# Performance work log

Hardware: AMD Instinct MI355X
Metric: run time of the kernel (lower is better)

The kernel has to match this reference:

```python
import jax, jax.numpy as jnp
from jax import lax
import numpy as np


def _dilate3x3(img):
    # Faithful to torch: zero-pad by 1 (f.pad default), then 3x3 max over the
    # padded window (strel of ones => plain max, zeros from padding included).
    imgp = jnp.pad(img, ((0, 0), (0, 0), (1, 1), (1, 1)))
    return lax.reduce_window(imgp, -jnp.inf, lax.max,
                             (1, 1, 3, 3), (1, 1, 1, 1), 'VALID')


def setup_inputs() -> dict:
    key = jax.random.key(0)
    x = jax.random.normal(key, (32, 3, 512, 512), dtype=jnp.float32)
    return {"in_tensor": x, "n_pixels": 20}


def reference(in_tensor, n_pixels):
    # smoother = linspace(1, 0, n+1); smoother_diff = -diff => 1/n per step (linear)
    smoother = jnp.linspace(1.0, 0.0, n_pixels + 1)
    sdiff = (-jnp.diff(smoother)).astype(in_tensor.dtype)  # [n_pixels]

    def step(carry, w):
        out, img = carry
        out = out + w * img
        img = _dilate3x3(img)
        return (out, img), None

    init = (jnp.zeros_like(in_tensor), in_tensor)
    (out, _), _ = lax.scan(step, init, sdiff)
    return out
```

## Files before the change

### kernel.cpp

```cpp
#include <hip/hip_runtime.h>

#define IMG_W 512
#define IMG_H 512
#define TILE 88
#define HALO 20
#define NSTEP 19
#define RH 8
#define RW 8
#define REG 128

__device__ __forceinline__ float max3f(float a, float b, float c) {
    return fmaxf(fmaxf(a, b), c);
}

__device__ __forceinline__ float dpp_shr1(float v) {
    int i = __builtin_bit_cast(int, v);
    i = __builtin_amdgcn_update_dpp(0, i, 0x111, 0xf, 0xf, true);
    return __builtin_bit_cast(float, i);
}
__device__ __forceinline__ float dpp_shl1(float v) {
    int i = __builtin_bit_cast(int, v);
    i = __builtin_amdgcn_update_dpp(0, i, 0x101, 0xf, 0xf, true);
    return __builtin_bit_cast(float, i);
}
__device__ __forceinline__ float bperm(int byteAddr, float v) {
    int i = __builtin_amdgcn_ds_bpermute(byteAddr, __builtin_bit_cast(int, v));
    return __builtin_bit_cast(float, i);
}

__device__ __forceinline__ void hrow(const float (&Ar)[RW], float (&h)[RW]) {
    float hl = dpp_shr1(Ar[RW - 1]);
    float hr = dpp_shl1(Ar[0]);
    h[0] = max3f(hl, Ar[0], Ar[1]);
    #pragma unroll
    for (int c = 1; c < RW - 1; ++c) h[c] = max3f(Ar[c - 1], Ar[c], Ar[c + 1]);
    h[RW - 1] = max3f(Ar[RW - 2], Ar[RW - 1], hr);
}

template<bool XM, bool YM>
__device__ __forceinline__ void rowop(const float (&hm1)[RW], const float (&hc)[RW],
                                      const float (&hn)[RW], float (&Ar)[RW],
                                      float (&accr)[RW], const float (&colm)[RW],
                                      float rm, bool needR) {
    float v[RW];
    #pragma unroll
    for (int c = 0; c < RW; ++c) v[c] = max3f(hm1[c], hc[c], hn[c]);
    if (XM) {
        #pragma unroll
        for (int c = 0; c < RW; ++c) v[c] *= colm[c];
    }
    if (YM) {
        if (needR) {
            #pragma unroll
            for (int c = 0; c < RW; ++c) v[c] *= rm;
        }
    }
    #pragma unroll
    for (int c = 0; c < RW; ++c) { Ar[c] = v[c]; accr[c] += v[c]; }
}

template<bool XM, bool YM>
__device__ __forceinline__ void body(const float* __restrict__ xc, float* __restrict__ oc,
                                     int gx0, int gy0, int tx, int ty, int lane,
                                     float4 (*botR)[4][16][2], float4 (*topR)[4][16][2]) {
    const int rx = tx * RW;
    const int ry = ty * RH;
    const int gx = gx0 + rx;
    const int gy = gy0 + ry;

    float A[RH][RW];
    float acc[RH][RW];
    float colm[RW], rowm[RH];
    bool needR = false;

    if (XM) {
        #pragma unroll
        for (int c = 0; c < RW; ++c) {
            int xx = gx + c;
            colm[c] = (xx >= 0 && xx < IMG_W) ? 1.f : 0.f;
        }
    }
    if (YM) {
        #pragma unroll
        for (int r = 0; r < RH; ++r) {
            int yy = gy + r;
            rowm[r] = (yy >= 0 && yy < IMG_H) ? 1.f : 0.f;
        }
        needR = (gy < 0) || (gy + RH > IMG_H);
    }

    if (XM || YM) {
        const bool fullin = (gx >= 0) && (gx + RW <= IMG_W) && (gy >= 0) && (gy + RH <= IMG_H);
        if (fullin) {
            #pragma unroll
            for (int r = 0; r < RH; ++r) {
                const float4* rp = (const float4*)(xc + (size_t)(gy + r) * IMG_W + gx);
                float4 v0 = rp[0], v1 = rp[1];
                A[r][0] = v0.x; A[r][1] = v0.y; A[r][2] = v0.z; A[r][3] = v0.w;
                A[r][4] = v1.x; A[r][5] = v1.y; A[r][6] = v1.z; A[r][7] = v1.w;
            }
        } else {
            #pragma unroll
            for (int r = 0; r < RH; ++r) {
                const int yr = gy + r;
                const int yy = min(max(yr, 0), IMG_H - 1);
                float rmv = (yr >= 0 && yr < IMG_H) ? 1.f : 0.f;
                const float* rp = xc + (size_t)yy * IMG_W;
                #pragma unroll
                for (int c = 0; c < RW; ++c) {
                    const int xr = gx + c;
                    const int xx = min(max(xr, 0), IMG_W - 1);
                    float m = rmv;
                    if (XM) m *= colm[c];
                    A[r][c] = rp[xx] * m;
                }
            }
        }
    } else {
        #pragma unroll
        for (int r = 0; r < RH; ++r) {
            const float4* rp = (const float4*)(xc + (size_t)(gy + r) * IMG_W + gx);
            float4 v0 = rp[0], v1 = rp[1];
            A[r][0] = v0.x; A[r][1] = v0.y; A[r][2] = v0.z; A[r][3] = v0.w;
            A[r][4] = v1.x; A[r][5] = v1.y; A[r][6] = v1.z; A[r][7] = v1.w;
        }
    }
    #pragma unroll
    for (int r = 0; r < RH; ++r) {
        #pragma unroll
        for (int c = 0; c < RW; ++c) acc[r][c] = A[r][c];
    }

    const int upA = ((lane - 16) & 63) << 2;
    const int dnA = ((lane + 16) & 63) << 2;
    const int gq = ty >> 2;
    const int tw = ty & 3;

    #pragma unroll 1
    for (int s = 0; s < NSTEP; ++s) {
        float hc[RW], h7[RW];
        hrow(A[0], hc);
        hrow(A[RH - 1], h7);
        float hm1[RW], hbot[RW];
        #pragma unroll
        for (int c = 0; c < RW; ++c) hm1[c] = bperm(upA, h7[c]);
        #pragma unroll
        for (int c = 0; c < RW; ++c) hbot[c] = bperm(dnA, hc[c]);

        const int buf = s & 1;
        if (tw == 3) {
            botR[buf][gq][tx][0] = make_float4(h7[0], h7[1], h7[2], h7[3]);
            botR[buf][gq][tx][1] = make_float4(h7[4], h7[5], h7[6], h7[7]);
        } else if (tw == 0) {
            topR[buf][gq][tx][0] = make_float4(hc[0], hc[1], hc[2], hc[3]);
            topR[buf][gq][tx][1] = make_float4(hc[4], hc[5], hc[6], hc[7]);
        }
        __syncthreads();
        if (tw == 0) {
            if (gq > 0) {
                float4 u0 = botR[buf][gq - 1][tx][0], u1 = botR[buf][gq - 1][tx][1];
                hm1[0] = u0.x; hm1[1] = u0.y; hm1[2] = u0.z; hm1[3] = u0.w;
                hm1[4] = u1.x; hm1[5] = u1.y; hm1[6] = u1.z; hm1[7] = u1.w;
            }
        } else if (tw == 3) {
            if (gq < 3) {
                float4 d0 = topR[buf][gq + 1][tx][0], d1 = topR[buf][gq + 1][tx][1];
                hbot[0] = d0.x; hbot[1] = d0.y; hbot[2] = d0.z; hbot[3] = d0.w;
                hbot[4] = d1.x; hbot[5] = d1.y; hbot[6] = d1.z; hbot[7] = d1.w;
            }
        }

        float h1[RW]; hrow(A[1], h1);
        float h2[RW]; hrow(A[2], h2);
        rowop<XM, YM>(hc, h1, h2, A[1], acc[1], colm, YM ? rowm[1] : 1.f, needR);
        rowop<XM, YM>(hm1, hc, h1, A[0], acc[0], colm, YM ? rowm[0] : 1.f, needR);
        float h3[RW]; hrow(A[3], h3);
        rowop<XM, YM>(h1, h2, h3, A[2], acc[2], colm, YM ? rowm[2] : 1.f, needR);
        float h4[RW]; hrow(A[4], h4);
        rowop<XM, YM>(h2, h3, h4, A[3], acc[3], colm, YM ? rowm[3] : 1.f, needR);
        float h5[RW]; hrow(A[5], h5);
        rowop<XM, YM>(h3, h4, h5, A[4], acc[4], colm, YM ? rowm[4] : 1.f, needR);
        float h6[RW]; hrow(A[6], h6);
        rowop<XM, YM>(h4, h5, h6, A[5], acc[5], colm, YM ? rowm[5] : 1.f, needR);
        rowop<XM, YM>(h5, h6, h7, A[6], acc[6], colm, YM ? rowm[6] : 1.f, needR);
        rowop<XM, YM>(h6, h7, hbot, A[7], acc[7], colm, YM ? rowm[7] : 1.f, needR);
    }

    if (XM || YM) {
        #pragma unroll
        for (int r = 0; r < RH; ++r) {
            const int rr = ry + r;
            const int yy = gy0 + rr;
            if (rr >= HALO && rr < HALO + TILE && yy < IMG_H) {
                #pragma unroll
                for (int c = 0; c < RW; ++c) {
                    const int cc = rx + c;
                    const int xx = gx0 + cc;
                    if (cc >= HALO && cc < HALO + TILE && xx < IMG_W)
                        oc[(size_t)yy * IMG_W + xx] = 0.05f * acc[r][c];
                }
            }
        }
    } else {
        #pragma unroll
        for (int r = 0; r < RH; ++r) {
            const int rr = ry + r;
            if (rr < HALO || rr >= HALO + TILE) continue;
            const int yy = gy0 + rr;
            float* rowp = oc + (size_t)yy * IMG_W + gx;
            if (tx >= 3 && tx <= 12) {
                ((float4*)rowp)[0] = make_float4(0.05f * acc[r][0], 0.05f * acc[r][1],
                                                 0.05f * acc[r][2], 0.05f * acc[r][3]);
                ((float4*)rowp)[1] = make_float4(0.05f * acc[r][4], 0.05f * acc[r][5],
                                                 0.05f * acc[r][6], 0.05f * acc[r][7]);
            } else if (tx == 2) {
                ((float4*)rowp)[1] = make_float4(0.05f * acc[r][4], 0.05f * acc[r][5],
                                                 0.05f * acc[r][6], 0.05f * acc[r][7]);
            } else if (tx == 13) {
                ((float4*)rowp)[0] = make_float4(0.05f * acc[r][0], 0.05f * acc[r][1],
                                                 0.05f * acc[r][2], 0.05f * acc[r][3]);
            }
        }
    }
}

__global__ __launch_bounds__(256, 2)
void blur_outwards_kernel(const float* __restrict__ x, float* __restrict__ out) {
    __shared__ float4 botR[2][4][16][2];
    __shared__ float4 topR[2][4][16][2];

    const int tid = threadIdx.x;
    const int tx = tid & 15;
    const int ty = tid >> 4;
    const int lane = tid & 63;

    const int ch  = blockIdx.z;
    const int gx0 = (int)blockIdx.x * TILE - HALO;
    const int gy0 = (int)blockIdx.y * TILE - HALO;

    const float* __restrict__ xc = x + (size_t)ch * (IMG_W * IMG_H);
    float* __restrict__ oc = out + (size_t)ch * (IMG_W * IMG_H);

    const bool xe = (gx0 < 0) || (gx0 + REG > IMG_W);
    const bool ye = (gy0 < 0) || (gy0 + REG > IMG_H);
    if (!xe && !ye)      body<false, false>(xc, oc, gx0, gy0, tx, ty, lane, botR, topR);
    else if (xe && !ye)  body<true,  false>(xc, oc, gx0, gy0, tx, ty, lane, botR, topR);
    else if (!xe && ye)  body<false, true >(xc, oc, gx0, gy0, tx, ty, lane, botR, topR);
    else                 body<true,  true >(xc, oc, gx0, gy0, tx, ty, lane, botR, topR);
}

extern "C" void kernel_launch(void* const* d_in, const int* in_sizes, int n_in,
                              void* d_out, int out_size, void* d_ws, size_t ws_size,
                              hipStream_t stream) {
    const float* x = (const float*)d_in[0];
    float* out = (float*)d_out;
    dim3 grid((IMG_W + TILE - 1) / TILE,
              (IMG_H + TILE - 1) / TILE,
              96);
    blur_outwards_kernel<<<grid, 256, 0, stream>>>(x, out);
}
```

Measured before the change: 313.9 us.

## Fuse two dilation steps per halo exchange to halve barriers and shuffles

Each loop iteration now exchanges a two-row halo (raw rows instead of horizontal maxima) and applies two 3x3 dilations back to back in registers, followed by one final single-step dilation, so 19 steps become 9 double steps plus 1. This halves the number of __syncthreads and halo exchange rounds. In exchange it does extra bpermutes and LDS traffic per round, recomputes the horizontal max for the halo rows, and adds register pressure from the larger halo buffers, which could reduce occupancy under the 2-blocks bound.

New measurement: 406.1 us. 29.4% more time.

```diff
diff --git a/kernel.cpp b/kernel.cpp
--- a/kernel.cpp
+++ b/kernel.cpp
@@ -4,7 +4,7 @@
 #define IMG_H 512
 #define TILE 88
 #define HALO 20
-#define NSTEP 19
+#define NSUP 9
 #define RH 8
 #define RW 8
 #define REG 128
@@ -38,31 +38,93 @@
 }
 
 template<bool XM, bool YM>
-__device__ __forceinline__ void rowop(const float (&hm1)[RW], const float (&hc)[RW],
-                                      const float (&hn)[RW], float (&Ar)[RW],
-                                      float (&accr)[RW], const float (&colm)[RW],
-                                      float rm, bool needR) {
-    float v[RW];
-    #pragma unroll
-    for (int c = 0; c < RW; ++c) v[c] = max3f(hm1[c], hc[c], hn[c]);
+__device__ __forceinline__ void drow(const float (&ha)[RW], const float (&hb)[RW],
+                                     const float (&hc)[RW], float (&d)[RW],
+                                     const float (&colm)[RW], float rm, bool needR) {
+    #pragma unroll
+    for (int c = 0; c < RW; ++c) d[c] = max3f(ha[c], hb[c], hc[c]);
     if (XM) {
         #pragma unroll
-        for (int c = 0; c < RW; ++c) v[c] *= colm[c];
+        for (int c = 0; c < RW; ++c) d[c] *= colm[c];
     }
     if (YM) {
         if (needR) {
             #pragma unroll
-            for (int c = 0; c < RW; ++c) v[c] *= rm;
-        }
-    }
-    #pragma unroll
-    for (int c = 0; c < RW; ++c) { Ar[c] = v[c]; accr[c] += v[c]; }
+            for (int c = 0; c < RW; ++c) d[c] *= rm;
+        }
+    }
+}
+
+template<bool XM, bool YM>
+__device__ __forceinline__ void dil2(float (&A)[RH][RW], float (&acc)[RH][RW],
+        const float (&Am2)[RW], const float (&Am1)[RW],
+        const float (&Ap8)[RW], const float (&Ap9)[RW],
+        const float (&colm)[RW], const float (&rowm)[RH],
+        float rmm1, float rm8, bool needR)
+{
+    float h1[3][RW], h2[3][RW];
+    hrow(A[0], h1[0]);
+    hrow(Am2, h1[1]);
+    hrow(Am1, h1[2]);
+    #pragma unroll
+    for (int i = 0; i <= 9; ++i) {
+        if (i >= 1) {
+            if (i <= 7)      hrow(A[i], h1[i % 3]);
+            else if (i == 8) hrow(Ap8, h1[2]);
+            else             hrow(Ap9, h1[0]);
+        }
+        {
+            const int rr = i - 1;
+            const int sa = (rr + 2) % 3;
+            const int sb = (rr + 3) % 3;
+            const int sc = i % 3;
+            float D1[RW];
+            const float rmv = YM ? ((rr == -1) ? rmm1
+                                  : ((rr == 8) ? rm8
+                                  : rowm[(rr >= 0 && rr <= 7) ? rr : 0])) : 1.f;
+            drow<XM, YM>(h1[sa], h1[sb], h1[sc], D1, colm, rmv, needR);
+            if (rr >= 0 && rr <= 7) {
+                #pragma unroll
+                for (int c = 0; c < RW; ++c) acc[rr][c] += D1[c];
+            }
+            hrow(D1, h2[sb]);
+        }
+        if (i >= 2) {
+            const int rd = i - 2;
+            const int sa = (rd + 2) % 3, sb = rd % 3, sc = (rd + 1) % 3;
+            float D2[RW];
+            drow<XM, YM>(h2[sa], h2[sb], h2[sc], D2, colm, YM ? rowm[rd] : 1.f, needR);
+            #pragma unroll
+            for (int c = 0; c < RW; ++c) { A[rd][c] = D2[c]; acc[rd][c] += D2[c]; }
+        }
+    }
+}
+
+template<bool XM, bool YM>
+__device__ __forceinline__ void dil1(float (&A)[RH][RW], float (&acc)[RH][RW],
+        const float (&Am1)[RW], const float (&Ap8)[RW],
+        const float (&colm)[RW], const float (&rowm)[RH], bool needR)
+{
+    float h[3][RW];
+    hrow(A[0], h[0]);
+    hrow(Am1, h[2]);
+    #pragma unroll
+    for (int i = 1; i <= 8; ++i) {
+        if (i <= 7) hrow(A[i], h[i % 3]);
+        else        hrow(Ap8, h[2]);
+        const int rd = i - 1;
+        const int sa = (rd + 2) % 3, sb = rd % 3, sc = i % 3;
+        float D[RW];
+        drow<XM, YM>(h[sa], h[sb], h[sc], D, colm, YM ? rowm[rd] : 1.f, needR);
+        #pragma unroll
+        for (int c = 0; c < RW; ++c) { A[rd][c] = D[c]; acc[rd][c] += D[c]; }
+    }
 }
 
 template<bool XM, bool YM>
 __device__ __forceinline__ void body(const float* __restrict__ xc, float* __restrict__ oc,
                                      int gx0, int gy0, int tx, int ty, int lane,
-                                     float4 (*botR)[4][16][2], float4 (*topR)[4][16][2]) {
+                                     float4 (*botR)[4][16][2][2], float4 (*topR)[4][16][2][2]) {
     const int rx = tx * RW;
     const int ry = ty * RH;
     const int gx = gx0 + rx;
@@ -71,7 +133,8 @@
     float A[RH][RW];
     float acc[RH][RW];
     float colm[RW], rowm[RH];
-    bool needR = false;
+    float rmm1 = 1.f, rm8 = 1.f;
+    bool needR = false, needRE = false;
 
     if (XM) {
         #pragma unroll
@@ -86,7 +149,10 @@
             int yy = gy + r;
             rowm[r] = (yy >= 0 && yy < IMG_H) ? 1.f : 0.f;
         }
-        needR = (gy < 0) || (gy + RH > IMG_H);
+        rmm1 = (gy - 1 >= 0 && gy - 1 < IMG_H) ? 1.f : 0.f;
+        rm8  = (gy + 8 >= 0 && gy + 8 < IMG_H) ? 1.f : 0.f;
+        needR  = (gy < 0) || (gy + RH > IMG_H);
+        needRE = (gy <= 0) || (gy + RH + 1 > IMG_H);
     }
 
     if (XM || YM) {
@@ -137,53 +203,80 @@
     const int tw = ty & 3;
 
     #pragma unroll 1
-    for (int s = 0; s < NSTEP; ++s) {
-        float hc[RW], h7[RW];
-        hrow(A[0], hc);
-        hrow(A[RH - 1], h7);
-        float hm1[RW], hbot[RW];
-        #pragma unroll
-        for (int c = 0; c < RW; ++c) hm1[c] = bperm(upA, h7[c]);
-        #pragma unroll
-        for (int c = 0; c < RW; ++c) hbot[c] = bperm(dnA, hc[c]);
-
-        const int buf = s & 1;
+    for (int t = 0; t < NSUP; ++t) {
+        float Am2[RW], Am1[RW], Ap8[RW], Ap9[RW];
+        #pragma unroll
+        for (int c = 0; c < RW; ++c) {
+            Am2[c] = bperm(upA, A[6][c]);
+            Am1[c] = bperm(upA, A[7][c]);
+            Ap8[c] = bperm(dnA, A[0][c]);
+            Ap9[c] = bperm(dnA, A[1][c]);
+        }
+        const int buf = t & 1;
         if (tw == 3) {
-            botR[buf][gq][tx][0] = make_float4(h7[0], h7[1], h7[2], h7[3]);
-            botR[buf][gq][tx][1] = make_float4(h7[4], h7[5], h7[6], h7[7]);
+            botR[buf][gq][tx][0][0] = make_float4(A[6][0], A[6][1], A[6][2], A[6][3]);
+            botR[buf][gq][tx][0][1] = make_float4(A[6][4], A[6][5], A[6][6], A[6][7]);
+            botR[buf][gq][tx][1][0] = make_float4(A[7][0], A[7][1], A[7][2], A[7][3]);
+            botR[buf][gq][tx][1][1] = make_float4(A[7][4], A[7][5], A[7][6], A[7][7]);
         } else if (tw == 0) {
-            topR[buf][gq][tx][0] = make_float4(hc[0], hc[1], hc[2], hc[3]);
-            topR[buf][gq][tx][1] = make_float4(hc[4], hc[5], hc[6], hc[7]);
+            topR[buf][gq][tx][0][0] = make_float4(A[0][0], A[0][1], A[0][2], A[0][3]);
+            topR[buf][gq][tx][0][1] = make_float4(A[0][4], A[0][5], A[0][6], A[0][7]);
+            topR[buf][gq][tx][1][0] = make_float4(A[1][0], A[1][1], A[1][2], A[1][3]);
+            topR[buf][gq][tx][1][1] = make_float4(A[1][4], A[1][5], A[1][6], A[1][7]);
         }
         __syncthreads();
         if (tw == 0) {
             if (gq > 0) {
-                float4 u0 = botR[buf][gq - 1][tx][0], u1 = botR[buf][gq - 1][tx][1];
-                hm1[0] = u0.x; hm1[1] = u0.y; hm1[2] = u0.z; hm1[3] = u0.w;
-                hm1[4] = u1.x; hm1[5] = u1.y; hm1[6] = u1.z; hm1[7] = u1.w;
+                float4 a0 = botR[buf][gq - 1][tx][0][0], a1 = botR[buf][gq - 1][tx][0][1];
+                float4 b0 = botR[buf][gq - 1][tx][1][0], b1 = botR[buf][gq - 1][tx][1][1];
+                Am2[0] = a0.x; Am2[1] = a0.y; Am2[2] = a0.z; Am2[3] = a0.w;
+                Am2[4] = a1.x; Am2[5] = a1.y; Am2[6] = a1.z; Am2[7] = a1.w;
+                Am1[0] = b0.x; Am1[1] = b0.y; Am1[2] = b0.z; Am1[3] = b0.w;
+                Am1[4] = b1.x; Am1[5] = b1.y; Am1[6] = b1.z; Am1[7] = b1.w;
             }
         } else if (tw == 3) {
             if (gq < 3) {
-                float4 d0 = topR[buf][gq + 1][tx][0], d1 = topR[buf][gq + 1][tx][1];
-                hbot[0] = d0.x; hbot[1] = d0.y; hbot[2] = d0.z; hbot[3] = d0.w;
-                hbot[4] = d1.x; hbot[5] = d1.y; hbot[6] = d1.z; hbot[7] = d1.w;
-            }
-        }
-
-        float h1[RW]; hrow(A[1], h1);
-        float h2[RW]; hrow(A[2], h2);
-        rowop<XM, YM>(hc, h1, h2, A[1], acc[1], colm, YM ? rowm[1] : 1.f, needR);
-        rowop<XM, YM>(hm1, hc, h1, A[0], acc[0], colm, YM ? rowm[0] : 1.f, needR);
-        float h3[RW]; hrow(A[3], h3);
-        rowop<XM, YM>(h1, h2, h3, A[2], acc[2], colm, YM ? rowm[2] : 1.f, needR);
-        float h4[RW]; hrow(A[4], h4);
-        rowop<XM, YM>(h2, h3, h4, A[3], acc[3], colm, YM ? rowm[3] : 1.f, needR);
-        float h5[RW]; hrow(A[5], h5);
-        rowop<XM, YM>(h3, h4, h5, A[4], acc[4], colm, YM ? rowm[4] : 1.f, needR);
-        float h6[RW]; hrow(A[6], h6);
-        rowop<XM, YM>(h4, h5, h6, A[5], acc[5], colm, YM ? rowm[5] : 1.f, needR);
-        rowop<XM, YM>(h5, h6, h7, A[6], acc[6], colm, YM ? rowm[6] : 1.f, needR);
-        rowop<XM, YM>(h6, h7, hbot, A[7], acc[7], colm, YM ? rowm[7] : 1.f, needR);
+                float4 a0 = topR[buf][gq + 1][tx][0][0], a1 = topR[buf][gq + 1][tx][0][1];
+                float4 b0 = topR[buf][gq + 1][tx][1][0], b1 = topR[buf][gq + 1][tx][1][1];
+                Ap8[0] = a0.x; Ap8[1] = a0.y; Ap8[2] = a0.z; Ap8[3] = a0.w;
+                Ap8[4] = a1.x; Ap8[5] = a1.y; Ap8[6] = a1.z; Ap8[7] = a1.w;
+                Ap9[0] = b0.x; Ap9[1] = b0.y; Ap9[2] = b0.z; Ap9[3] = b0.w;
+                Ap9[4] = b1.x; Ap9[5] = b1.y; Ap9[6] = b1.z; Ap9[7] = b1.w;
+            }
+        }
+        dil2<XM, YM>(A, acc, Am2, Am1, Ap8, Ap9, colm, rowm, rmm1, rm8, needRE);
+    }
+
+    {
+        float Am1[RW], Ap8[RW];
+        #pragma unroll
+        for (int c = 0; c < RW; ++c) {
+            Am1[c] = bperm(upA, A[7][c]);
+            Ap8[c] = bperm(dnA, A[0][c]);
+        }
+        const int buf = NSUP & 1;
+        if (tw == 3) {
+            botR[buf][gq][tx][1][0] = make_float4(A[7][0], A[7][1], A[7][2], A[7][3]);
+            botR[buf][gq][tx][1][1] = make_float4(A[7][4], A[7][5], A[7][6], A[7][7]);
+        } else if (tw == 0) {
+            topR[buf][gq][tx][0][0] = make_float4(A[0][0], A[0][1], A[0][2], A[0][3]);
+            topR[buf][gq][tx][0][1] = make_float4(A[0][4], A[0][5], A[0][6], A[0][7]);
+        }
+        __syncthreads();
+        if (tw == 0) {
+            if (gq > 0) {
+                float4 b0 = botR[buf][gq - 1][tx][1][0], b1 = botR[buf][gq - 1][tx][1][1];
+                Am1[0] = b0.x; Am1[1] = b0.y; Am1[2] = b0.z; Am1[3] = b0.w;
+                Am1[4] = b1.x; Am1[5] = b1.y; Am1[6] = b1.z; Am1[7] = b1.w;
+            }
+        } else if (tw == 3) {
+            if (gq < 3) {
+                float4 a0 = topR[buf][gq + 1][tx][0][0], a1 = topR[buf][gq + 1][tx][0][1];
+                Ap8[0] = a0.x; Ap8[1] = a0.y; Ap8[2] = a0.z; Ap8[3] = a0.w;
+                Ap8[4] = a1.x; Ap8[5] = a1.y; Ap8[6] = a1.z; Ap8[7] = a1.w;
+            }
+        }
+        dil1<XM, YM>(A, acc, Am1, Ap8, colm, rowm, needR);
     }
 
     if (XM || YM) {
@@ -226,8 +319,8 @@
 
 __global__ __launch_bounds__(256, 2)
 void blur_outwards_kernel(const float* __restrict__ x, float* __restrict__ out) {
-    __shared__ float4 botR[2][4][16][2];
-    __shared__ float4 topR[2][4][16][2];
+    __shared__ float4 botR[2][4][16][2][2];
+    __shared__ float4 topR[2][4][16][2][2];
 
     const int tid = threadIdx.x;
     const int tx = tid & 15;
```
